# Performance work log

Measured on AMD Instinct MI355X. Metric: run time of the kernel, lower is better.

The kernel has to match this reference:

```python
import jax, jax.numpy as jnp
import numpy as np

IN_F, OUT_F = 4096, 4096
TD_X, TD_Y = 16, 16
L, K, V = 16, 2, 1
HS, GS = 128, 128          # hadamard_size, group_size
NB = (OUT_F // TD_X) * (IN_F // TD_Y)   # 65536 weight tiles
NBITS = TD_X * TD_Y * K                 # 512 bits per tile (tail-biting stream)
T = TD_X * TD_Y // V                    # 256 decoded states per tile


def _hadamard(n):
    H = np.array([[1.0]], dtype=np.float32)
    while H.shape[0] < n:
        H = np.block([[H, H], [H, -H]])
    return jnp.asarray(H / np.sqrt(np.float32(n)))


def setup_inputs() -> dict:
    key = jax.random.key(0)
    k1, k2, k3, k4 = jax.random.split(key, 4)
    inp = jax.random.normal(k1, (4, 2048, IN_F), dtype=jnp.float32)
    # packed trellis: 32 words x 16 bits = 512 bits per tile
    trellis = jax.random.randint(k2, (NB, NBITS // 16), 0, 65536, dtype=jnp.int32)
    tlut = jax.random.normal(k3, (2 ** 16, V), dtype=jnp.float32) * 0.05
    scales = jax.random.uniform(k4, (OUT_F * IN_F // GS, 1), dtype=jnp.float32, minval=0.5, maxval=1.5)
    return {"input": inp, "trellis": trellis, "tlut": tlut, "scales": scales}


def _decode_weights(trellis, tlut, scales):
    # unpack 16-bit words into a per-tile bitstream, MSB first -> (NB, 512)
    bits = ((trellis[:, :, None] >> (15 - jnp.arange(16, dtype=jnp.int32))) & 1).reshape(NB, NBITS)
    # bitshift trellis: state i is the L-bit window starting at bit i*K (circular)
    pos = jnp.arange(T, dtype=jnp.int32) * K
    state = jnp.zeros((NB, T), dtype=jnp.int32)
    for j in range(L):  # fixed small loop over window bits
        state = state * 2 + bits[:, (pos + j) % NBITS]
    vals = tlut[state].reshape(NB, TD_X, TD_Y)  # LUT decode, V=1
    W = vals.reshape(OUT_F // TD_X, IN_F // TD_Y, TD_X, TD_Y)
    W = W.transpose(0, 2, 1, 3).reshape(OUT_F, IN_F)
    # per-group scales, row-major groups of GS along in_features
    return (W.reshape(-1, GS) * scales).reshape(OUT_F, IN_F)


def reference(input, trellis, tlut, scales):
    H = _hadamard(HS)
    # rotate activations into the hadamard domain (per group of HS features)
    x = (input.reshape(*input.shape[:-1], IN_F // HS, HS) @ H).reshape(input.shape)
    W = _decode_weights(trellis, tlut, scales)  # [out, in]
    return x @ W.T
```

## Files before the change

kernel.cpp:

```cpp
#include <hip/hip_runtime.h>
#include <hip/hip_bf16.h>
#include <stdint.h>

#define MROWS 8192
#define K_TOT 4096
#define N_TOT 4096

typedef __attribute__((ext_vector_type(8))) short bf16x8;
typedef __attribute__((ext_vector_type(4))) float f32x4;
typedef __attribute__((ext_vector_type(8))) unsigned short ushort8;

#define GLB(p) ((const __attribute__((address_space(1))) void*)(p))
#define LDSP(p) ((__attribute__((address_space(3))) void*)(p))

#define CONV_BLOCKS 16384
#define DEC_BLOCKS  2048

__global__ __launch_bounds__(256) void prep_k(const float* __restrict__ in,
                                              const int* __restrict__ trellis,
                                              const float* __restrict__ tlut,
                                              const float* __restrict__ scales,
                                              __hip_bfloat16* __restrict__ xb,
                                              __hip_bfloat16* __restrict__ wb) {
    const int tid = threadIdx.x;
    if (blockIdx.x < CONV_BLOCKS) {
        const long base = ((long)blockIdx.x * 256 + tid) * 8;
        float4 x0 = *(const float4*)(in + base);
        float4 x1 = *(const float4*)(in + base + 4);
        ushort8 u;
        __hip_bfloat16 h;
        h = __float2bfloat16(x0.x); u[0] = *(unsigned short*)&h;
        h = __float2bfloat16(x0.y); u[1] = *(unsigned short*)&h;
        h = __float2bfloat16(x0.z); u[2] = *(unsigned short*)&h;
        h = __float2bfloat16(x0.w); u[3] = *(unsigned short*)&h;
        h = __float2bfloat16(x1.x); u[4] = *(unsigned short*)&h;
        h = __float2bfloat16(x1.y); u[5] = *(unsigned short*)&h;
        h = __float2bfloat16(x1.z); u[6] = *(unsigned short*)&h;
        h = __float2bfloat16(x1.w); u[7] = *(unsigned short*)&h;
        *(ushort8*)((unsigned short*)xb + base) = u;
    } else {
        __shared__ uint32_t sw[1024];
        __shared__ __hip_bfloat16 Hs[128 * 136];
        const int b = blockIdx.x - CONV_BLOCKS;
        const int tbx = b >> 3;
        const int g0 = (b & 7) * 4;
        {
            int4 v = *((const int4*)(trellis + ((long)tbx * 256 + g0 * 8) * 32) + tid);
            sw[tid * 4 + 0] = (uint32_t)v.x & 0xFFFFu;
            sw[tid * 4 + 1] = (uint32_t)v.y & 0xFFFFu;
            sw[tid * 4 + 2] = (uint32_t)v.z & 0xFFFFu;
            sw[tid * 4 + 3] = (uint32_t)v.w & 0xFFFFu;
        }
        {
            const int n = tid >> 1;
            const int k0 = (tid & 1) * 64;
            const unsigned short pos = 0x3F80, neg = 0xBF80;
#pragma unroll 8
            for (int k = 0; k < 64; k++) {
                unsigned short s = (__popc(n & (k0 + k)) & 1) ? neg : pos;
                *((unsigned short*)Hs + n * 136 + k0 + k) = s;
            }
        }
        __syncthreads();

        const int wave = tid >> 6;
        const int lane = tid & 63;
        const int m = lane & 15;
        const int quad = lane >> 4;
        const int g = g0 + wave;

        bf16x8 af[4];
#pragma unroll
        for (int kc = 0; kc < 4; kc++) {
            float v[8];
#pragma unroll
            for (int j = 0; j < 8; j++) {
                const int k = kc * 32 + quad * 8 + j;
                const int tile = wave * 8 + (k >> 4);
                const int c = k & 15;
                const int t = m * 16 + c;
                const int q = t >> 3;
                const int rb = (c & 7) * 2;
                const uint32_t w0 = sw[tile * 32 + q];
                const uint32_t w1 = sw[tile * 32 + ((q + 1) & 31)];
                const uint32_t st = ((w0 << rb) | (w1 >> (16 - rb))) & 0xFFFFu;
                v[j] = tlut[st];
            }
#pragma unroll
            for (int j = 0; j < 8; j++) {
                __hip_bfloat16 h = __float2bfloat16(v[j]);
                af[kc][j] = *(short*)&h;
            }
        }
        float scl[4];
#pragma unroll
        for (int r = 0; r < 4; r++)
            scl[r] = scales[(tbx * 16 + quad * 4 + r) * 32 + g] * 0.088388347648318447f;

#pragma unroll
        for (int nt = 0; nt < 8; nt++) {
            f32x4 c = {};
#pragma unroll
            for (int kc = 0; kc < 4; kc++) {
                bf16x8 bf = *(const bf16x8*)&Hs[(nt * 16 + m) * 136 + kc * 32 + quad * 8];
                c = __builtin_amdgcn_mfma_f32_16x16x32_bf16(af[kc], bf, c, 0, 0, 0);
            }
            const long col = (long)g * 128 + nt * 16 + m;
#pragma unroll
            for (int r = 0; r < 4; r++) {
                const long orow = tbx * 16 + quad * 4 + r;
                wb[orow * K_TOT + col] = __float2bfloat16(c[r] * scl[r]);
            }
        }
    }
}

#define BK 32
#define NTILES (K_TOT / BK)
#define BUFSZ 32768

__global__ __launch_bounds__(512, 2) void gemm_k(const __hip_bfloat16* __restrict__ A,
                                                 const __hip_bfloat16* __restrict__ B,
                                                 float* __restrict__ C) {
    __shared__ __align__(16) char sbuf[4 * BUFSZ];
    const int tid  = threadIdx.x;
    const int wave = tid >> 6;
    const int lane = tid & 63;
    const long m0 = (long)blockIdx.y * 256;
    const long n0 = (long)blockIdx.x * 256;

    const int wm = wave >> 2;
    const int wn = wave & 3;

    const __hip_bfloat16* srcA[2];
    const __hip_bfloat16* srcB[2];
#pragma unroll
    for (int j = 0; j < 2; j++) {
        const int p   = j * 512 + tid;
        const int row = p >> 2;
        const int seg = (p & 3) ^ ((row >> 1) & 3);
        srcA[j] = A + (m0 + row) * K_TOT + seg * 8;
        srcB[j] = B + (n0 + row) * K_TOT + seg * 8;
    }
    const int ldsOff0 = wave * 1024;
    const int ldsOff1 = 8192 + wave * 1024;

    const int lr  = lane & 15;
    const int lq  = lane >> 4;
    const int xsw = (lq ^ ((lr >> 1) & 3)) * 16;
    const int arow0 = wm * 128 + lr;
    const int brow0 = wn * 64 + lr;

    f32x4 acc[8][4] = {};

#define STAGE(tt)                                                                         \
    do {                                                                                  \
        char* _b = (char*)sbuf + ((tt) & 3) * BUFSZ;                                      \
        const long _ko = (long)(tt) * BK;                                                 \
        __builtin_amdgcn_global_load_lds(GLB(srcA[0] + _ko), LDSP(_b + ldsOff0), 16, 0, 0);\
        __builtin_amdgcn_global_load_lds(GLB(srcA[1] + _ko), LDSP(_b + ldsOff1), 16, 0, 0);\
        __builtin_amdgcn_global_load_lds(GLB(srcB[0] + _ko), LDSP(_b + 16384 + ldsOff0), 16, 0, 0);\
        __builtin_amdgcn_global_load_lds(GLB(srcB[1] + _ko), LDSP(_b + 16384 + ldsOff1), 16, 0, 0);\
    } while (0)

    STAGE(0);
    STAGE(1);
    asm volatile("s_waitcnt vmcnt(4)" ::: "memory");
    __builtin_amdgcn_s_barrier();
    asm volatile("" ::: "memory");

    for (int t = 0; t < NTILES; ++t) {
        if (t + 2 < NTILES) STAGE(t + 2);

        const char* bufA = (const char*)sbuf + (t & 3) * BUFSZ;
        const char* bufB = bufA + 16384;

        bf16x8 bfr[4], af[4];
#pragma unroll
        for (int j = 0; j < 4; j++)
            bfr[j] = *(const bf16x8*)(bufB + (brow0 + j * 16) * 64 + xsw);
#pragma unroll
        for (int i = 0; i < 4; i++)
            af[i] = *(const bf16x8*)(bufA + (arow0 + i * 16) * 64 + xsw);

        __builtin_amdgcn_s_setprio(1);
#pragma unroll
        for (int i = 0; i < 4; i++)
#pragma unroll
            for (int j = 0; j < 4; j++)
                acc[i][j] = __builtin_amdgcn_mfma_f32_16x16x32_bf16(af[i], bfr[j], acc[i][j], 0, 0, 0);
        __builtin_amdgcn_s_setprio(0);

#pragma unroll
        for (int i = 0; i < 4; i++)
            af[i] = *(const bf16x8*)(bufA + (arow0 + (i + 4) * 16) * 64 + xsw);

        __builtin_amdgcn_s_setprio(1);
#pragma unroll
        for (int i = 0; i < 4; i++)
#pragma unroll
            for (int j = 0; j < 4; j++)
                acc[i + 4][j] = __builtin_amdgcn_mfma_f32_16x16x32_bf16(af[i], bfr[j], acc[i + 4][j], 0, 0, 0);
        __builtin_amdgcn_s_setprio(0);

        if (t + 1 < NTILES) {
            if (t + 2 < NTILES) asm volatile("s_waitcnt vmcnt(4)" ::: "memory");
            else                asm volatile("s_waitcnt vmcnt(0)" ::: "memory");
            __builtin_amdgcn_s_barrier();
            asm volatile("" ::: "memory");
        }
    }
#undef STAGE

#pragma unroll
    for (int i = 0; i < 8; i++)
#pragma unroll
        for (int j = 0; j < 4; j++) {
            const long m = m0 + wm * 128 + i * 16 + lq * 4;
            const long n = n0 + wn * 64 + j * 16 + lr;
            float* cp = C + m * N_TOT + n;
#pragma unroll
            for (int r = 0; r < 4; r++)
                cp[(long)r * N_TOT] = acc[i][j][r];
        }
}

extern "C" void kernel_launch(void* const* d_in, const int* in_sizes, int n_in,
                              void* d_out, int out_size, void* d_ws, size_t ws_size,
                              hipStream_t stream) {
    const float* inp     = (const float*)d_in[0];
    const int*   trellis = (const int*)d_in[1];
    const float* tlut    = (const float*)d_in[2];
    const float* scales  = (const float*)d_in[3];
    float* out = (float*)d_out;

    __hip_bfloat16* xb = (__hip_bfloat16*)d_ws;
    __hip_bfloat16* wb = xb + (size_t)MROWS * K_TOT;

    hipLaunchKernelGGL(prep_k, dim3(CONV_BLOCKS + DEC_BLOCKS), dim3(256), 0, stream,
                       inp, trellis, tlut, scales, xb, wb);
    hipLaunchKernelGGL(gemm_k, dim3(N_TOT / 256, MROWS / 256), dim3(512), 0, stream, xb, wb, out);
}
```

Measured before the change: 507.9 us.

## Split prep kernel, swizzle GEMM block order, and interleave staged loads with MFMA phases

Splits the combined conversion/decode prep kernel into two separate kernels, so the conversion blocks no longer reserve the decode path's large LDS allocation. The GEMM remaps block IDs with an XCD-style swizzle to improve L2 locality across chiplets. It also splits the per-step global-to-LDS staging into A and B halves, issued between the two MFMA phases with extra barriers, to spread memory traffic across the step. The extra barriers per K step add synchronization cost and could reduce overlap.

```diff
diff --git a/kernel.cpp b/kernel.cpp
--- a/kernel.cpp
+++ b/kernel.cpp
@@ -16,132 +16,133 @@
 #define CONV_BLOCKS 16384
 #define DEC_BLOCKS  2048
 
-__global__ __launch_bounds__(256) void prep_k(const float* __restrict__ in,
-                                              const int* __restrict__ trellis,
-                                              const float* __restrict__ tlut,
-                                              const float* __restrict__ scales,
-                                              __hip_bfloat16* __restrict__ xb,
-                                              __hip_bfloat16* __restrict__ wb) {
+__global__ __launch_bounds__(256) void conv_k(const float* __restrict__ in,
+                                              __hip_bfloat16* __restrict__ xb) {
     const int tid = threadIdx.x;
-    if (blockIdx.x < CONV_BLOCKS) {
-        const long base = ((long)blockIdx.x * 256 + tid) * 8;
-        float4 x0 = *(const float4*)(in + base);
-        float4 x1 = *(const float4*)(in + base + 4);
-        ushort8 u;
-        __hip_bfloat16 h;
-        h = __float2bfloat16(x0.x); u[0] = *(unsigned short*)&h;
-        h = __float2bfloat16(x0.y); u[1] = *(unsigned short*)&h;
-        h = __float2bfloat16(x0.z); u[2] = *(unsigned short*)&h;
-        h = __float2bfloat16(x0.w); u[3] = *(unsigned short*)&h;
-        h = __float2bfloat16(x1.x); u[4] = *(unsigned short*)&h;
-        h = __float2bfloat16(x1.y); u[5] = *(unsigned short*)&h;
-        h = __float2bfloat16(x1.z); u[6] = *(unsigned short*)&h;
-        h = __float2bfloat16(x1.w); u[7] = *(unsigned short*)&h;
-        *(ushort8*)((unsigned short*)xb + base) = u;
-    } else {
-        __shared__ uint32_t sw[1024];
-        __shared__ __hip_bfloat16 Hs[128 * 136];
-        const int b = blockIdx.x - CONV_BLOCKS;
-        const int tbx = b >> 3;
-        const int g0 = (b & 7) * 4;
-        {
-            int4 v = *((const int4*)(trellis + ((long)tbx * 256 + g0 * 8) * 32) + tid);
-            sw[tid * 4 + 0] = (uint32_t)v.x & 0xFFFFu;
-            sw[tid * 4 + 1] = (uint32_t)v.y & 0xFFFFu;
-            sw[tid * 4 + 2] = (uint32_t)v.z & 0xFFFFu;
-            sw[tid * 4 + 3] = (uint32_t)v.w & 0xFFFFu;
-        }
-        {
-            const int n = tid >> 1;
-            const int k0 = (tid & 1) * 64;
-            const unsigned short pos = 0x3F80, neg = 0xBF80;
+    const long base = ((long)blockIdx.x * 256 + tid) * 8;
+    float4 x0 = *(const float4*)(in + base);
+    float4 x1 = *(const float4*)(in + base + 4);
+    ushort8 u;
+    __hip_bfloat16 h;
+    h = __float2bfloat16(x0.x); u[0] = *(unsigned short*)&h;
+    h = __float2bfloat16(x0.y); u[1] = *(unsigned short*)&h;
+    h = __float2bfloat16(x0.z); u[2] = *(unsigned short*)&h;
+    h = __float2bfloat16(x0.w); u[3] = *(unsigned short*)&h;
+    h = __float2bfloat16(x1.x); u[4] = *(unsigned short*)&h;
+    h = __float2bfloat16(x1.y); u[5] = *(unsigned short*)&h;
+    h = __float2bfloat16(x1.z); u[6] = *(unsigned short*)&h;
+    h = __float2bfloat16(x1.w); u[7] = *(unsigned short*)&h;
+    *(ushort8*)((unsigned short*)xb + base) = u;
+}
+
+__global__ __launch_bounds__(256) void dec_k(const int* __restrict__ trellis,
+                                             const float* __restrict__ tlut,
+                                             const float* __restrict__ scales,
+                                             __hip_bfloat16* __restrict__ wb) {
+    __shared__ uint32_t sw[1024];
+    __shared__ __hip_bfloat16 Hs[128 * 136];
+    const int tid = threadIdx.x;
+    const int b = blockIdx.x;
+    const int tbx = b >> 3;
+    const int g0 = (b & 7) * 4;
+    {
+        int4 v = *((const int4*)(trellis + ((long)tbx * 256 + g0 * 8) * 32) + tid);
+        sw[tid * 4 + 0] = (uint32_t)v.x & 0xFFFFu;
+        sw[tid * 4 + 1] = (uint32_t)v.y & 0xFFFFu;
+        sw[tid * 4 + 2] = (uint32_t)v.z & 0xFFFFu;
+        sw[tid * 4 + 3] = (uint32_t)v.w & 0xFFFFu;
+    }
+    {
+        const int n = tid >> 1;
+        const int k0 = (tid & 1) * 64;
+        const unsigned short pos = 0x3F80, neg = 0xBF80;
 #pragma unroll 8
-            for (int k = 0; k < 64; k++) {
-                unsigned short s = (__popc(n & (k0 + k)) & 1) ? neg : pos;
-                *((unsigned short*)Hs + n * 136 + k0 + k) = s;
-            }
-        }
-        __syncthreads();
-
-        const int wave = tid >> 6;
-        const int lane = tid & 63;
-        const int m = lane & 15;
-        const int quad = lane >> 4;
-        const int g = g0 + wave;
-
-        bf16x8 af[4];
+        for (int k = 0; k < 64; k++) {
+            unsigned short s = (__popc(n & (k0 + k)) & 1) ? neg : pos;
+            *((unsigned short*)Hs + n * 136 + k0 + k) = s;
+        }
+    }
+    __syncthreads();
+
+    const int wave = tid >> 6;
+    const int lane = tid & 63;
+    const int m = lane & 15;
+    const int quad = lane >> 4;
+    const int g = g0 + wave;
+
+    bf16x8 af[4];
+#pragma unroll
+    for (int kc = 0; kc < 4; kc++) {
+        float v[8];
+#pragma unroll
+        for (int j = 0; j < 8; j++) {
+            const int k = kc * 32 + quad * 8 + j;
+            const int tile = wave * 8 + (k >> 4);
+            const int c = k & 15;
+            const int t = m * 16 + c;
+            const int q = t >> 3;
+            const int rb = (c & 7) * 2;
+            const uint32_t w0 = sw[tile * 32 + q];
+            const uint32_t w1 = sw[tile * 32 + ((q + 1) & 31)];
+            const uint32_t st = ((w0 << rb) | (w1 >> (16 - rb))) & 0xFFFFu;
+            v[j] = tlut[st];
+        }
+#pragma unroll
+        for (int j = 0; j < 8; j++) {
+            __hip_bfloat16 h = __float2bfloat16(v[j]);
+            af[kc][j] = *(short*)&h;
+        }
+    }
+    float scl[4];
+#pragma unroll
+    for (int r = 0; r < 4; r++)
+        scl[r] = scales[(tbx * 16 + quad * 4 + r) * 32 + g] * 0.088388347648318447f;
+
+#pragma unroll
+    for (int nt = 0; nt < 8; nt++) {
+        f32x4 c = {};
 #pragma unroll
         for (int kc = 0; kc < 4; kc++) {
-            float v[8];
-#pragma unroll
-            for (int j = 0; j < 8; j++) {
-                const int k = kc * 32 + quad * 8 + j;
-                const int tile = wave * 8 + (k >> 4);
-                const int c = k & 15;
-                const int t = m * 16 + c;
-                const int q = t >> 3;
-                const int rb = (c & 7) * 2;
-                const uint32_t w0 = sw[tile * 32 + q];
-                const uint32_t w1 = sw[tile * 32 + ((q + 1) & 31)];
-                const uint32_t st = ((w0 << rb) | (w1 >> (16 - rb))) & 0xFFFFu;
-                v[j] = tlut[st];
-            }
-#pragma unroll
-            for (int j = 0; j < 8; j++) {
-                __hip_bfloat16 h = __float2bfloat16(v[j]);
-                af[kc][j] = *(short*)&h;
-            }
-        }
-        float scl[4];
-#pragma unroll
-        for (int r = 0; r < 4; r++)
-            scl[r] = scales[(tbx * 16 + quad * 4 + r) * 32 + g] * 0.088388347648318447f;
-
-#pragma unroll
-        for (int nt = 0; nt < 8; nt++) {
-            f32x4 c = {};
-#pragma unroll
-            for (int kc = 0; kc < 4; kc++) {
-                bf16x8 bf = *(const bf16x8*)&Hs[(nt * 16 + m) * 136 + kc * 32 + quad * 8];
-                c = __builtin_amdgcn_mfma_f32_16x16x32_bf16(af[kc], bf, c, 0, 0, 0);
-            }
-            const long col = (long)g * 128 + nt * 16 + m;
-#pragma unroll
-            for (int r = 0; r < 4; r++) {
-                const long orow = tbx * 16 + quad * 4 + r;
-                wb[orow * K_TOT + col] = __float2bfloat16(c[r] * scl[r]);
-            }
+            bf16x8 bf = *(const bf16x8*)&Hs[(nt * 16 + m) * 136 + kc * 32 + quad * 8];
+            c = __builtin_amdgcn_mfma_f32_16x16x32_bf16(af[kc], bf, c, 0, 0, 0);
+        }
+        const long col = (long)g * 128 + nt * 16 + m;
+#pragma unroll
+        for (int r = 0; r < 4; r++) {
+            const long orow = tbx * 16 + quad * 4 + r;
+            wb[orow * K_TOT + col] = __float2bfloat16(c[r] * scl[r]);
         }
     }
 }
 
 #define BK 32
-#define NTILES (K_TOT / BK)
-#define BUFSZ 32768
+#define NSTEPS (K_TOT / BK)
+#define SLOT_SZ 32768
 
 __global__ __launch_bounds__(512, 2) void gemm_k(const __hip_bfloat16* __restrict__ A,
                                                  const __hip_bfloat16* __restrict__ B,
                                                  float* __restrict__ C) {
-    __shared__ __align__(16) char sbuf[4 * BUFSZ];
+    __shared__ __align__(16) char sbuf[4 * SLOT_SZ];
     const int tid  = threadIdx.x;
     const int wave = tid >> 6;
     const int lane = tid & 63;
-    const long m0 = (long)blockIdx.y * 256;
-    const long n0 = (long)blockIdx.x * 256;
+
+    const int bid  = (int)blockIdx.y * (N_TOT / 256) + (int)blockIdx.x;
+    const int sbid = (bid & 7) * 64 + (bid >> 3);
+    const long m0 = (long)(sbid >> 4) * 256;
+    const long n0 = (long)(sbid & 15) * 256;
 
     const int wm = wave >> 2;
     const int wn = wave & 3;
 
-    const __hip_bfloat16* srcA[2];
-    const __hip_bfloat16* srcB[2];
-#pragma unroll
-    for (int j = 0; j < 2; j++) {
-        const int p   = j * 512 + tid;
-        const int row = p >> 2;
-        const int seg = (p & 3) ^ ((row >> 1) & 3);
-        srcA[j] = A + (m0 + row) * K_TOT + seg * 8;
-        srcB[j] = B + (n0 + row) * K_TOT + seg * 8;
-    }
+    const int p0 = tid, p1 = 512 + tid;
+    const int r0 = p0 >> 2, r1 = p1 >> 2;
+    const int sg0 = (p0 & 3) ^ ((r0 >> 1) & 3);
+    const int sg1 = (p1 & 3) ^ ((r1 >> 1) & 3);
+    const __hip_bfloat16* srcA0 = A + (m0 + r0) * K_TOT + sg0 * 8;
+    const __hip_bfloat16* srcA1 = A + (m0 + r1) * K_TOT + sg1 * 8;
+    const __hip_bfloat16* srcB0 = B + (n0 + r0) * K_TOT + sg0 * 8;
+    const __hip_bfloat16* srcB1 = B + (n0 + r1) * K_TOT + sg1 * 8;
     const int ldsOff0 = wave * 1024;
     const int ldsOff1 = 8192 + wave * 1024;
 
@@ -153,64 +154,76 @@
 
     f32x4 acc[8][4] = {};
 
-#define STAGE(tt)                                                                         \
-    do {                                                                                  \
-        char* _b = (char*)sbuf + ((tt) & 3) * BUFSZ;                                      \
-        const long _ko = (long)(tt) * BK;                                                 \
-        __builtin_amdgcn_global_load_lds(GLB(srcA[0] + _ko), LDSP(_b + ldsOff0), 16, 0, 0);\
-        __builtin_amdgcn_global_load_lds(GLB(srcA[1] + _ko), LDSP(_b + ldsOff1), 16, 0, 0);\
-        __builtin_amdgcn_global_load_lds(GLB(srcB[0] + _ko), LDSP(_b + 16384 + ldsOff0), 16, 0, 0);\
-        __builtin_amdgcn_global_load_lds(GLB(srcB[1] + _ko), LDSP(_b + 16384 + ldsOff1), 16, 0, 0);\
+#define STAGE_A(ss)                                                                        \
+    do {                                                                                   \
+        char* _b = (char*)sbuf + ((ss) & 3) * SLOT_SZ;                                     \
+        const long _ko = (long)(ss) * BK;                                                  \
+        __builtin_amdgcn_global_load_lds(GLB(srcA0 + _ko), LDSP(_b + ldsOff0), 16, 0, 0);  \
+        __builtin_amdgcn_global_load_lds(GLB(srcA1 + _ko), LDSP(_b + ldsOff1), 16, 0, 0);  \
     } while (0)
-
-    STAGE(0);
-    STAGE(1);
+#define STAGE_B(ss)                                                                        \
+    do {                                                                                   \
+        char* _b = (char*)sbuf + ((ss) & 3) * SLOT_SZ + 16384;                             \
+        const long _ko = (long)(ss) * BK;                                                  \
+        __builtin_amdgcn_global_load_lds(GLB(srcB0 + _ko), LDSP(_b + ldsOff0), 16, 0, 0);  \
+        __builtin_amdgcn_global_load_lds(GLB(srcB1 + _ko), LDSP(_b + ldsOff1), 16, 0, 0);  \
+    } while (0)
+
+    STAGE_A(0); STAGE_B(0);
+    STAGE_A(1); STAGE_B(1);
     asm volatile("s_waitcnt vmcnt(4)" ::: "memory");
     __builtin_amdgcn_s_barrier();
     asm volatile("" ::: "memory");
 
-    for (int t = 0; t < NTILES; ++t) {
-        if (t + 2 < NTILES) STAGE(t + 2);
-
-        const char* bufA = (const char*)sbuf + (t & 3) * BUFSZ;
+    for (int s = 0; s < NSTEPS; ++s) {
+        const char* bufA = (const char*)sbuf + (s & 3) * SLOT_SZ;
         const char* bufB = bufA + 16384;
 
-        bf16x8 bfr[4], af[4];
+        bf16x8 bfr[4], afA[4], afB[4];
 #pragma unroll
         for (int j = 0; j < 4; j++)
             bfr[j] = *(const bf16x8*)(bufB + (brow0 + j * 16) * 64 + xsw);
 #pragma unroll
         for (int i = 0; i < 4; i++)
-            af[i] = *(const bf16x8*)(bufA + (arow0 + i * 16) * 64 + xsw);
+            afA[i] = *(const bf16x8*)(bufA + (arow0 + i * 16) * 64 + xsw);
+        if (s + 2 < NSTEPS) STAGE_A(s + 2);
+        __builtin_amdgcn_s_barrier();
+        asm volatile("" ::: "memory");
 
         __builtin_amdgcn_s_setprio(1);
 #pragma unroll
         for (int i = 0; i < 4; i++)
 #pragma unroll
             for (int j = 0; j < 4; j++)
-                acc[i][j] = __builtin_amdgcn_mfma_f32_16x16x32_bf16(af[i], bfr[j], acc[i][j], 0, 0, 0);
+                acc[i][j] = __builtin_amdgcn_mfma_f32_16x16x32_bf16(afA[i], bfr[j], acc[i][j], 0, 0, 0);
         __builtin_amdgcn_s_setprio(0);
-
-#pragma unroll
-        for (int i = 0; i < 4; i++)
-            af[i] = *(const bf16x8*)(bufA + (arow0 + (i + 4) * 16) * 64 + xsw);
+        __builtin_amdgcn_s_barrier();
+        asm volatile("" ::: "memory");
+
+#pragma unroll
+        for (int i = 0; i < 4; i++)
+            afB[i] = *(const bf16x8*)(bufA + (arow0 + (i + 4) * 16) * 64 + xsw);
+        if (s + 2 < NSTEPS) STAGE_B(s + 2);
+        __builtin_amdgcn_s_barrier();
+        asm volatile("" ::: "memory");
 
         __builtin_amdgcn_s_setprio(1);
 #pragma unroll
         for (int i = 0; i < 4; i++)
 #pragma unroll
             for (int j = 0; j < 4; j++)
-                acc[i + 4][j] = __builtin_amdgcn_mfma_f32_16x16x32_bf16(af[i], bfr[j], acc[i + 4][j], 0, 0, 0);
+                acc[i + 4][j] = __builtin_amdgcn_mfma_f32_16x16x32_bf16(afB[i], bfr[j], acc[i + 4][j], 0, 0, 0);
         __builtin_amdgcn_s_setprio(0);
 
-        if (t + 1 < NTILES) {
-            if (t + 2 < NTILES) asm volatile("s_waitcnt vmcnt(4)" ::: "memory");
-            else                asm volatile("s_waitcnt vmcnt(0)" ::: "memory");
+        if (s + 2 < NSTEPS)      asm volatile("s_waitcnt vmcnt(4)" ::: "memory");
+        else if (s + 1 < NSTEPS) asm volatile("s_waitcnt vmcnt(0)" ::: "memory");
+        if (s + 1 < NSTEPS) {
             __builtin_amdgcn_s_barrier();
             asm volatile("" ::: "memory");
         }
     }
-#undef STAGE
+#undef STAGE_A
+#undef STAGE_B
 
 #pragma unroll
     for (int i = 0; i < 8; i++)
@@ -237,7 +250,7 @@
     __hip_bfloat16* xb = (__hip_bfloat16*)d_ws;
     __hip_bfloat16* wb = xb + (size_t)MROWS * K_TOT;
 
-    hipLaunchKernelGGL(prep_k, dim3(CONV_BLOCKS + DEC_BLOCKS), dim3(256), 0, stream,
-                       inp, trellis, tlut, scales, xb, wb);
+    hipLaunchKernelGGL(conv_k, dim3(CONV_BLOCKS), dim3(256), 0, stream, inp, xb);
+    hipLaunchKernelGGL(dec_k, dim3(DEC_BLOCKS), dim3(256), 0, stream, trellis, tlut, scales, wb);
     hipLaunchKernelGGL(gemm_k, dim3(N_TOT / 256, MROWS / 256), dim3(512), 0, stream, xb, wb, out);
 }
```

New measurement: 522.7 us. +2.9%, slower.

## Split prep kernel and stage bf16 LUT in shared memory for weight decode

Applied to the files above, without the earlier changes.

Splits the combined conversion/decode kernel into separate conv and decode kernels. The decode kernel now uses 512 threads per block, covers 8 groups per block, and first copies the whole 64K-entry LUT into shared memory as bf16, so state lookups become LDS reads instead of scattered global loads. Hadamard B fragments are generated in registers with popcount parity instead of being read from a shared-memory matrix. The trade-off is that each block reloads 256KB of LUT from global memory, and the 128KB LDS footprint limits occupancy to one block per CU. It also adds an extra kernel launch.

```diff
diff --git a/kernel.cpp b/kernel.cpp
--- a/kernel.cpp
+++ b/kernel.cpp
@@ -9,108 +9,112 @@
 typedef __attribute__((ext_vector_type(8))) short bf16x8;
 typedef __attribute__((ext_vector_type(4))) float f32x4;
 typedef __attribute__((ext_vector_type(8))) unsigned short ushort8;
+typedef __attribute__((ext_vector_type(4))) unsigned short ushort4v;
 
 #define GLB(p) ((const __attribute__((address_space(1))) void*)(p))
 #define LDSP(p) ((__attribute__((address_space(3))) void*)(p))
 
 #define CONV_BLOCKS 16384
-#define DEC_BLOCKS  2048
-
-__global__ __launch_bounds__(256) void prep_k(const float* __restrict__ in,
-                                              const int* __restrict__ trellis,
-                                              const float* __restrict__ tlut,
-                                              const float* __restrict__ scales,
-                                              __hip_bfloat16* __restrict__ xb,
-                                              __hip_bfloat16* __restrict__ wb) {
+#define DEC_BLOCKS  1024
+
+__global__ __launch_bounds__(256) void conv_k(const float* __restrict__ in,
+                                              __hip_bfloat16* __restrict__ xb) {
     const int tid = threadIdx.x;
-    if (blockIdx.x < CONV_BLOCKS) {
-        const long base = ((long)blockIdx.x * 256 + tid) * 8;
-        float4 x0 = *(const float4*)(in + base);
-        float4 x1 = *(const float4*)(in + base + 4);
-        ushort8 u;
+    const long base = ((long)blockIdx.x * 256 + tid) * 8;
+    float4 x0 = *(const float4*)(in + base);
+    float4 x1 = *(const float4*)(in + base + 4);
+    ushort8 u;
+    __hip_bfloat16 h;
+    h = __float2bfloat16(x0.x); u[0] = *(unsigned short*)&h;
+    h = __float2bfloat16(x0.y); u[1] = *(unsigned short*)&h;
+    h = __float2bfloat16(x0.z); u[2] = *(unsigned short*)&h;
+    h = __float2bfloat16(x0.w); u[3] = *(unsigned short*)&h;
+    h = __float2bfloat16(x1.x); u[4] = *(unsigned short*)&h;
+    h = __float2bfloat16(x1.y); u[5] = *(unsigned short*)&h;
+    h = __float2bfloat16(x1.z); u[6] = *(unsigned short*)&h;
+    h = __float2bfloat16(x1.w); u[7] = *(unsigned short*)&h;
+    *(ushort8*)((unsigned short*)xb + base) = u;
+}
+
+__global__ __launch_bounds__(512) void dec_k(const int* __restrict__ trellis,
+                                             const float* __restrict__ tlut,
+                                             const float* __restrict__ scales,
+                                             __hip_bfloat16* __restrict__ wb) {
+    __shared__ unsigned short tl[65536];
+    __shared__ uint32_t sw[2048];
+    const int tid = threadIdx.x;
+    const int b = blockIdx.x;
+    const int tbx = b >> 2;
+    const int g0 = (b & 3) * 8;
+
+#pragma unroll
+    for (int it = 0; it < 32; ++it) {
+        const int idx = it * 2048 + tid * 4;
+        float4 f = *(const float4*)(tlut + idx);
+        ushort4v u;
         __hip_bfloat16 h;
-        h = __float2bfloat16(x0.x); u[0] = *(unsigned short*)&h;
-        h = __float2bfloat16(x0.y); u[1] = *(unsigned short*)&h;
-        h = __float2bfloat16(x0.z); u[2] = *(unsigned short*)&h;
-        h = __float2bfloat16(x0.w); u[3] = *(unsigned short*)&h;
-        h = __float2bfloat16(x1.x); u[4] = *(unsigned short*)&h;
-        h = __float2bfloat16(x1.y); u[5] = *(unsigned short*)&h;
-        h = __float2bfloat16(x1.z); u[6] = *(unsigned short*)&h;
-        h = __float2bfloat16(x1.w); u[7] = *(unsigned short*)&h;
-        *(ushort8*)((unsigned short*)xb + base) = u;
-    } else {
-        __shared__ uint32_t sw[1024];
-        __shared__ __hip_bfloat16 Hs[128 * 136];
-        const int b = blockIdx.x - CONV_BLOCKS;
-        const int tbx = b >> 3;
-        const int g0 = (b & 7) * 4;
-        {
-            int4 v = *((const int4*)(trellis + ((long)tbx * 256 + g0 * 8) * 32) + tid);
-            sw[tid * 4 + 0] = (uint32_t)v.x & 0xFFFFu;
-            sw[tid * 4 + 1] = (uint32_t)v.y & 0xFFFFu;
-            sw[tid * 4 + 2] = (uint32_t)v.z & 0xFFFFu;
-            sw[tid * 4 + 3] = (uint32_t)v.w & 0xFFFFu;
-        }
-        {
-            const int n = tid >> 1;
-            const int k0 = (tid & 1) * 64;
-            const unsigned short pos = 0x3F80, neg = 0xBF80;
-#pragma unroll 8
-            for (int k = 0; k < 64; k++) {
-                unsigned short s = (__popc(n & (k0 + k)) & 1) ? neg : pos;
-                *((unsigned short*)Hs + n * 136 + k0 + k) = s;
-            }
-        }
-        __syncthreads();
-
-        const int wave = tid >> 6;
-        const int lane = tid & 63;
-        const int m = lane & 15;
-        const int quad = lane >> 4;
-        const int g = g0 + wave;
-
-        bf16x8 af[4];
+        h = __float2bfloat16(f.x); u[0] = *(unsigned short*)&h;
+        h = __float2bfloat16(f.y); u[1] = *(unsigned short*)&h;
+        h = __float2bfloat16(f.z); u[2] = *(unsigned short*)&h;
+        h = __float2bfloat16(f.w); u[3] = *(unsigned short*)&h;
+        *(ushort4v*)&tl[idx] = u;
+    }
+    {
+        int4 v = *((const int4*)(trellis + ((long)tbx * 256 + g0 * 8) * 32) + tid);
+        sw[tid * 4 + 0] = (uint32_t)v.x & 0xFFFFu;
+        sw[tid * 4 + 1] = (uint32_t)v.y & 0xFFFFu;
+        sw[tid * 4 + 2] = (uint32_t)v.z & 0xFFFFu;
+        sw[tid * 4 + 3] = (uint32_t)v.w & 0xFFFFu;
+    }
+    __syncthreads();
+
+    const int wave = tid >> 6;
+    const int lane = tid & 63;
+    const int m = lane & 15;
+    const int quad = lane >> 4;
+    const int g = g0 + wave;
+
+    bf16x8 af[4];
+#pragma unroll
+    for (int kc = 0; kc < 4; kc++) {
+#pragma unroll
+        for (int j = 0; j < 8; j++) {
+            const int k = kc * 32 + quad * 8 + j;
+            const int tile = wave * 8 + (k >> 4);
+            const int c = k & 15;
+            const int t = m * 16 + c;
+            const int q = t >> 3;
+            const int rb = (c & 7) * 2;
+            const uint32_t w0 = sw[tile * 32 + q];
+            const uint32_t w1 = sw[tile * 32 + ((q + 1) & 31)];
+            const uint32_t st = ((w0 << rb) | (w1 >> (16 - rb))) & 0xFFFFu;
+            af[kc][j] = (short)tl[st];
+        }
+    }
+    float scl[4];
+#pragma unroll
+    for (int r = 0; r < 4; r++)
+        scl[r] = scales[(tbx * 16 + quad * 4 + r) * 32 + g] * 0.088388347648318447f;
+
+#pragma unroll
+    for (int nt = 0; nt < 8; nt++) {
+        f32x4 c = {};
+        const int n = nt * 16 + m;
 #pragma unroll
         for (int kc = 0; kc < 4; kc++) {
-            float v[8];
+            bf16x8 bf;
 #pragma unroll
             for (int j = 0; j < 8; j++) {
                 const int k = kc * 32 + quad * 8 + j;
-                const int tile = wave * 8 + (k >> 4);
-                const int c = k & 15;
-                const int t = m * 16 + c;
-                const int q = t >> 3;
-                const int rb = (c & 7) * 2;
-                const uint32_t w0 = sw[tile * 32 + q];
-                const uint32_t w1 = sw[tile * 32 + ((q + 1) & 31)];
-                const uint32_t st = ((w0 << rb) | (w1 >> (16 - rb))) & 0xFFFFu;
-                v[j] = tlut[st];
+                bf[j] = (short)((__popc(n & k) & 1) ? 0xBF80 : 0x3F80);
             }
-#pragma unroll
-            for (int j = 0; j < 8; j++) {
-                __hip_bfloat16 h = __float2bfloat16(v[j]);
-                af[kc][j] = *(short*)&h;
-            }
-        }
-        float scl[4];
-#pragma unroll
-        for (int r = 0; r < 4; r++)
-            scl[r] = scales[(tbx * 16 + quad * 4 + r) * 32 + g] * 0.088388347648318447f;
-
-#pragma unroll
-        for (int nt = 0; nt < 8; nt++) {
-            f32x4 c = {};
-#pragma unroll
-            for (int kc = 0; kc < 4; kc++) {
-                bf16x8 bf = *(const bf16x8*)&Hs[(nt * 16 + m) * 136 + kc * 32 + quad * 8];
-                c = __builtin_amdgcn_mfma_f32_16x16x32_bf16(af[kc], bf, c, 0, 0, 0);
-            }
-            const long col = (long)g * 128 + nt * 16 + m;
-#pragma unroll
-            for (int r = 0; r < 4; r++) {
-                const long orow = tbx * 16 + quad * 4 + r;
-                wb[orow * K_TOT + col] = __float2bfloat16(c[r] * scl[r]);
-            }
+            c = __builtin_amdgcn_mfma_f32_16x16x32_bf16(af[kc], bf, c, 0, 0, 0);
+        }
+        const long col = (long)g * 128 + nt * 16 + m;
+#pragma unroll
+        for (int r = 0; r < 4; r++) {
+            const long orow = tbx * 16 + quad * 4 + r;
+            wb[orow * K_TOT + col] = __float2bfloat16(c[r] * scl[r]);
         }
     }
 }
@@ -237,7 +241,7 @@
     __hip_bfloat16* xb = (__hip_bfloat16*)d_ws;
     __hip_bfloat16* wb = xb + (size_t)MROWS * K_TOT;
 
-    hipLaunchKernelGGL(prep_k, dim3(CONV_BLOCKS + DEC_BLOCKS), dim3(256), 0, stream,
-                       inp, trellis, tlut, scales, xb, wb);
+    hipLaunchKernelGGL(conv_k, dim3(CONV_BLOCKS), dim3(256), 0, stream, inp, xb);
+    hipLaunchKernelGGL(dec_k, dim3(DEC_BLOCKS), dim3(512), 0, stream, trellis, tlut, scales, wb);
     hipLaunchKernelGGL(gemm_k, dim3(N_TOT / 256, MROWS / 256), dim3(512), 0, stream, xb, wb, out);
 }
```

New measurement: 490.0 us. -3.5%, faster.
